# Performance work log

Hardware: AMD Instinct MI355X
Metric: run time of the kernel (lower is better)

Reference implementation:

```python
import jax, jax.numpy as jnp
import numpy as np

WS = 8      # window size
NH = 8      # num heads
DIM = 192


def _rel_coords_table(ws):
    c = np.arange(-(ws - 1), ws, dtype=np.float32)
    t = np.stack(np.meshgrid(c, c, indexing='ij'), axis=-1)  # (2ws-1, 2ws-1, 2)
    t = t / (ws - 1) * 8.0
    t = np.sign(t) * np.log2(np.abs(t) + 1.0) / np.log2(8.0)
    return jnp.asarray(t.reshape(-1, 2))


def _rel_pos_index(ws):
    coords = np.stack(np.meshgrid(np.arange(ws), np.arange(ws), indexing='ij'))  # (2,ws,ws)
    cf = coords.reshape(2, -1)
    rel = (cf[:, :, None] - cf[:, None, :]).transpose(1, 2, 0).astype(np.int64)  # (N,N,2)
    rel[..., 0] += ws - 1
    rel[..., 1] += ws - 1
    rel[..., 0] *= 2 * ws - 1
    return jnp.asarray(rel.sum(-1))  # (N,N)


_RCT = _rel_coords_table(WS)   # (225, 2)
_RPI = _rel_pos_index(WS)      # (64, 64)


def setup_inputs() -> dict:
    key = jax.random.key(0)
    ks = jax.random.split(key, 6)
    B, C, H, W = 4, DIM, 256, 256
    return {
        'x': jax.random.normal(ks[0], (B, C, H, W), dtype=jnp.float32),
        'img_alpha': jnp.ones((B, 1, H, W), dtype=jnp.float32),
        'qkv_w': jax.random.normal(ks[1], (3 * C, C), dtype=jnp.float32) * 0.02,
        'q_bias': jnp.zeros((C,), dtype=jnp.float32),
        'v_bias': jnp.zeros((C,), dtype=jnp.float32),
        'logit_scale': jnp.full((NH, 1, 1), np.log(10.0), dtype=jnp.float32),
        'cpb_w1': jax.random.normal(ks[2], (2, 512), dtype=jnp.float32) * 0.02,
        'cpb_b1': jnp.zeros((512,), dtype=jnp.float32),
        'cpb_w2': jax.random.normal(ks[3], (512, NH), dtype=jnp.float32) * 0.02,
        'proj_w': jax.random.normal(ks[4], (C, C), dtype=jnp.float32) * 0.02,
        'proj_b': jnp.zeros((C,), dtype=jnp.float32),
    }


def _forward(x, qkv_w, q_bias, v_bias, logit_scale, cpb_w1, cpb_b1, cpb_w2, proj_w, proj_b):
    B, C, H, W = x.shape
    ws, nh = WS, NH
    hd = C // nh
    # window partition: (B,C,H,W) -> (B*nW, N, C) with N = ws*ws
    xw = (x.transpose(0, 2, 3, 1)
           .reshape(B, H // ws, ws, W // ws, ws, C)
           .transpose(0, 1, 3, 2, 4, 5)
           .reshape(-1, ws * ws, C))
    Bw, N, _ = xw.shape
    # qkv with bias = [q_bias, 0, v_bias]
    qkv_b = jnp.concatenate([q_bias, jnp.zeros_like(v_bias), v_bias])
    qkv = (xw @ qkv_w.T + qkv_b).reshape(Bw, N, 3, nh, hd).transpose(2, 0, 3, 1, 4)
    q, k, v = qkv[0], qkv[1], qkv[2]  # (Bw, nh, N, hd)
    # cosine attention with clamped learnable logit scale
    qn = q / jnp.maximum(jnp.linalg.norm(q, axis=-1, keepdims=True), 1e-12)
    kn = k / jnp.maximum(jnp.linalg.norm(k, axis=-1, keepdims=True), 1e-12)
    scale = jnp.exp(jnp.minimum(logit_scale, jnp.log(jnp.float32(100.0))))  # (nh,1,1)
    attn = jnp.einsum('bhnd,bhmd->bhnm', qn, kn) * scale
    # relative position bias from small MLP + gather
    table = jax.nn.relu(_RCT @ cpb_w1 + cpb_b1) @ cpb_w2        # (225, nh)
    bias = table[_RPI.reshape(-1)].reshape(N, N, nh).transpose(2, 0, 1)  # (nh,N,N)
    bias = 16.0 * jax.nn.sigmoid(bias)
    attn = jax.nn.softmax(attn + bias[None], axis=-1)
    out = jnp.einsum('bhnm,bhmd->bhnd', attn, v).transpose(0, 2, 1, 3).reshape(Bw, N, C)
    out = out @ proj_w.T + proj_b
    # window reverse -> (B,C,H,W)
    out = (out.reshape(B, H // ws, W // ws, ws, ws, C)
              .transpose(0, 1, 3, 2, 4, 5)
              .reshape(B, H, W, C)
              .transpose(0, 3, 1, 2))
    return x + out  # residual (shortcut)


def reference(x, img_alpha, qkv_w, q_bias, v_bias, logit_scale,
              cpb_w1, cpb_b1, cpb_w2, proj_w, proj_b):
    # shift_size == 0: img_alpha only rides along through partition and is sliced off;
    # with all-ones alpha the zero-window removal is a no-op, so it does not affect output.
    del img_alpha
    return _forward(x, qkv_w, q_bias, v_bias, logit_scale,
                    cpb_w1, cpb_b1, cpb_w2, proj_w, proj_b)
```

## Files before the change

### kernel.cpp

```cpp
#include <hip/hip_runtime.h>

typedef unsigned short u16;
typedef __attribute__((ext_vector_type(8))) short bf16x8;
typedef __attribute__((ext_vector_type(4))) float f32x4;

#define C_    192
#define HW_   65536

__device__ inline u16 f2bf(float f) {
  union { float f; unsigned u; } x; x.f = f;
  unsigned r = x.u + 0x7FFFu + ((x.u >> 16) & 1u);
  return (u16)(r >> 16);
}
__device__ inline float bf2f(u16 s) {
  union { unsigned u; float f; } x; x.u = ((unsigned)s) << 16;
  return x.f;
}
__device__ inline unsigned pkbf(float lo, float hi) {
  unsigned r;
  asm("v_cvt_pk_bf16_f32 %0, %1, %2" : "=v"(r) : "v"(lo), "v"(hi));
  return r;
}

__global__ void k_convert(const float* __restrict__ qkv_w, const float* __restrict__ proj_w,
                          const float* __restrict__ q_bias, const float* __restrict__ v_bias,
                          u16* __restrict__ wq, u16* __restrict__ wp, float* __restrict__ qkvb) {
  int i = blockIdx.x * 256 + threadIdx.x;
  if (i < 110592) wq[i] = f2bf(qkv_w[i]);
  else if (i < 147456) wp[i - 110592] = f2bf(proj_w[i - 110592]);
  else if (i < 148032) {
    int j = i - 147456;
    qkvb[j] = (j < 192) ? q_bias[j] : ((j < 384) ? 0.f : v_bias[j - 384]);
  }
}

__global__ void k_table(const float* __restrict__ w1, const float* __restrict__ b1,
                        const float* __restrict__ w2, float* __restrict__ table) {
  int row = blockIdx.x;
  int tid = threadIdx.x;
  int a = row / 15, b = row % 15;
  float va = (float)(a - 7) * (8.0f / 7.0f);
  float vb = (float)(b - 7) * (8.0f / 7.0f);
  float c0 = copysignf(log2f(fabsf(va) + 1.0f) * (1.0f / 3.0f), va);
  float c1 = copysignf(log2f(fabsf(vb) + 1.0f) * (1.0f / 3.0f), vb);
  float acc[8];
#pragma unroll
  for (int o = 0; o < 8; ++o) acc[o] = 0.f;
  for (int k = tid; k < 512; k += 256) {
    float h = fmaxf(c0 * w1[k] + c1 * w1[512 + k] + b1[k], 0.f);
#pragma unroll
    for (int o = 0; o < 8; ++o) acc[o] += h * w2[k * 8 + o];
  }
  __shared__ float part[4][8];
  int wave = tid >> 6;
#pragma unroll
  for (int o = 0; o < 8; ++o) {
    float v = acc[o];
    v += __shfl_xor(v, 1, 64);  v += __shfl_xor(v, 2, 64);
    v += __shfl_xor(v, 4, 64);  v += __shfl_xor(v, 8, 64);
    v += __shfl_xor(v, 16, 64); v += __shfl_xor(v, 32, 64);
    acc[o] = v;
  }
  if ((tid & 63) == 0)
#pragma unroll
    for (int o = 0; o < 8; ++o) part[wave][o] = acc[o];
  __syncthreads();
  if (tid < 8)
    table[row * 8 + tid] = part[0][tid] + part[1][tid] + part[2][tid] + part[3][tid];
}

__global__ void k_biasfill(const float* __restrict__ table, float* __restrict__ bias3) {
  int p = blockIdx.x * 256 + threadIdx.x;
  int h = p >> 12, t = (p >> 6) & 63, g = (p >> 4) & 3, u = p & 15;
  int nt = u >> 2, r = u & 3;
  int s = nt * 16 + g * 4 + r;
  int idx = ((t >> 3) - (s >> 3) + 7) * 15 + ((t & 7) - (s & 7) + 7);
  float v = table[idx * 8 + h];
  bias3[p] = 16.0f / (1.0f + __expf(-v));
}

__device__ __forceinline__ void attn_window(
    u16* __restrict__ R0, u16* __restrict__ Sw, float* __restrict__ ikw,
    const u16* __restrict__ wq, const float* __restrict__ qkvb,
    const float* __restrict__ bias3,
    int h, int g, int li, float scaleh,
    const bf16x8* qw0, const bf16x8* qw1) {
  bf16x8 z8 = {0, 0, 0, 0, 0, 0, 0, 0};
  f32x4 zf = {0.f, 0.f, 0.f, 0.f};
  float iqr[4];
  bf16x8 qf[4], kf[4];

  {
    f32x4 cb0 = *(const f32x4*)(qkvb + h * 24 + g * 4);
    f32x4 cb1 = *(const f32x4*)(qkvb + h * 24 + 16 + g * 4);
#pragma unroll
    for (int tb = 0; tb < 4; ++tb) {
      int t = tb * 16 + li;
      bf16x8 xf[6];
#pragma unroll
      for (int ks = 0; ks < 6; ++ks)
        xf[ks] = *(const bf16x8*)&R0[t * 200 + ks * 32 + g * 8];
      f32x4 a0 = zf, a1 = zf;
#pragma unroll
      for (int ks = 0; ks < 6; ++ks) {
        a0 = __builtin_amdgcn_mfma_f32_16x16x32_bf16(qw0[ks], xf[ks], a0, 0, 0, 0);
        a1 = __builtin_amdgcn_mfma_f32_16x16x32_bf16(qw1[ks], xf[ks], a1, 0, 0, 0);
      }
      float p = 0.f;
#pragma unroll
      for (int r = 0; r < 4; ++r) { a0[r] += cb0[r]; p += a0[r] * a0[r]; }
      if (g < 2) {
#pragma unroll
        for (int r = 0; r < 4; ++r) { a1[r] += cb1[r]; p += a1[r] * a1[r]; }
      }
      p += __shfl_xor(p, 16, 64);
      p += __shfl_xor(p, 32, 64);
      iqr[tb] = __builtin_amdgcn_rsqf(fmaxf(p, 1e-24f)) * scaleh;
      uint2 pk;
      pk.x = pkbf(a0[0], a0[1]);
      pk.y = pkbf(a0[2], a0[3]);
      *(uint2*)&Sw[t * 24 + g * 4] = pk;
      if (g < 2) {
        pk.x = pkbf(a1[0], a1[1]);
        pk.y = pkbf(a1[2], a1[3]);
        *(uint2*)&Sw[t * 24 + 16 + g * 4] = pk;
      }
    }
  }

  bf16x8 kw0[6], kw1[6];
  {
    const u16* wr0 = wq + (size_t)(192 + h * 24 + li) * 192 + g * 8;
    const u16* wr1 = wq + (size_t)(192 + h * 24 + 16 + (li & 7)) * 192 + g * 8;
#pragma unroll
    for (int ks = 0; ks < 6; ++ks) {
      kw0[ks] = *(const bf16x8*)(wr0 + ks * 32);
      kw1[ks] = *(const bf16x8*)(wr1 + ks * 32);
    }
  }
#pragma unroll
  for (int tb = 0; tb < 4; ++tb)
    qf[tb] = (g < 3) ? *(const bf16x8*)&Sw[(tb * 16 + li) * 24 + g * 8] : z8;

  {
    f32x4 cb0 = *(const f32x4*)(qkvb + 192 + h * 24 + g * 4);
    f32x4 cb1 = *(const f32x4*)(qkvb + 192 + h * 24 + 16 + g * 4);
#pragma unroll
    for (int nt = 0; nt < 4; ++nt) {
      int t = nt * 16 + li;
      bf16x8 xf[6];
#pragma unroll
      for (int ks = 0; ks < 6; ++ks)
        xf[ks] = *(const bf16x8*)&R0[t * 200 + ks * 32 + g * 8];
      f32x4 a0 = zf, a1 = zf;
#pragma unroll
      for (int ks = 0; ks < 6; ++ks) {
        a0 = __builtin_amdgcn_mfma_f32_16x16x32_bf16(kw0[ks], xf[ks], a0, 0, 0, 0);
        a1 = __builtin_amdgcn_mfma_f32_16x16x32_bf16(kw1[ks], xf[ks], a1, 0, 0, 0);
      }
      float p = 0.f;
#pragma unroll
      for (int r = 0; r < 4; ++r) { a0[r] += cb0[r]; p += a0[r] * a0[r]; }
      if (g < 2) {
#pragma unroll
        for (int r = 0; r < 4; ++r) { a1[r] += cb1[r]; p += a1[r] * a1[r]; }
      }
      p += __shfl_xor(p, 16, 64);
      p += __shfl_xor(p, 32, 64);
      float ik = __builtin_amdgcn_rsqf(fmaxf(p, 1e-24f));
      if (g == 0) ikw[t] = ik;
      uint2 pk;
      pk.x = pkbf(a0[0], a0[1]);
      pk.y = pkbf(a0[2], a0[3]);
      *(uint2*)&Sw[t * 24 + g * 4] = pk;
      if (g < 2) {
        pk.x = pkbf(a1[0], a1[1]);
        pk.y = pkbf(a1[2], a1[3]);
        *(uint2*)&Sw[t * 24 + 16 + g * 4] = pk;
      }
    }
  }

  bf16x8 vw0[6], vw1[6];
  {
    const u16* wr0 = wq + (size_t)(384 + h * 24 + li) * 192 + g * 8;
    const u16* wr1 = wq + (size_t)(384 + h * 24 + 16 + (li & 7)) * 192 + g * 8;
#pragma unroll
    for (int ks = 0; ks < 6; ++ks) {
      vw0[ks] = *(const bf16x8*)(wr0 + ks * 32);
      vw1[ks] = *(const bf16x8*)(wr1 + ks * 32);
    }
  }
#pragma unroll
  for (int nt = 0; nt < 4; ++nt)
    kf[nt] = (g < 3) ? *(const bf16x8*)&Sw[(nt * 16 + li) * 24 + g * 8] : z8;

  {
    float vb0 = qkvb[384 + h * 24 + li];
    float vb1 = qkvb[384 + h * 24 + 16 + (li & 7)];
#pragma unroll
    for (int tb = 0; tb < 4; ++tb) {
      int t = tb * 16 + li;
      bf16x8 xf[6];
#pragma unroll
      for (int ks = 0; ks < 6; ++ks)
        xf[ks] = *(const bf16x8*)&R0[t * 200 + ks * 32 + g * 8];
      f32x4 a0 = zf, a1 = zf;
#pragma unroll
      for (int ks = 0; ks < 6; ++ks) {
        a0 = __builtin_amdgcn_mfma_f32_16x16x32_bf16(xf[ks], vw0[ks], a0, 0, 0, 0);
        a1 = __builtin_amdgcn_mfma_f32_16x16x32_bf16(xf[ks], vw1[ks], a1, 0, 0, 0);
      }
      uint2 pk;
      pk.x = pkbf(a0[0] + vb0, a0[1] + vb0);
      pk.y = pkbf(a0[2] + vb0, a0[3] + vb0);
      *(uint2*)&Sw[li * 72 + tb * 16 + g * 4] = pk;
      if (li < 8) {
        pk.x = pkbf(a1[0] + vb1, a1[1] + vb1);
        pk.y = pkbf(a1[2] + vb1, a1[3] + vb1);
        *(uint2*)&Sw[(16 + li) * 72 + tb * 16 + g * 4] = pk;
      }
    }
  }
  bf16x8 vf0[2], vf1[2];
#pragma unroll
  for (int ks = 0; ks < 2; ++ks) {
    vf0[ks] = *(const bf16x8*)&Sw[li * 72 + ks * 32 + g * 8];
    vf1[ks] = (li < 8) ? *(const bf16x8*)&Sw[(16 + li) * 72 + ks * 32 + g * 8] : z8;
  }

  f32x4 bx[2][4];
  {
    const float* bp0 = bias3 + ((h * 64 + li) << 6) + (g << 4);
#pragma unroll
    for (int nt = 0; nt < 4; ++nt) bx[0][nt] = *(const f32x4*)(bp0 + (nt << 2));
  }
#pragma unroll
  for (int tb = 0; tb < 4; ++tb) {
    if (tb < 3) {
      const float* bpn = bias3 + ((h * 64 + (tb + 1) * 16 + li) << 6) + (g << 4);
#pragma unroll
      for (int nt = 0; nt < 4; ++nt) bx[(tb + 1) & 1][nt] = *(const f32x4*)(bpn + (nt << 2));
    }
    f32x4 s4[4];
#pragma unroll
    for (int nt = 0; nt < 4; ++nt)
      s4[nt] = __builtin_amdgcn_mfma_f32_16x16x32_bf16(kf[nt], qf[tb], zf, 0, 0, 0);
    float iq = iqr[tb];
#pragma unroll
    for (int nt = 0; nt < 4; ++nt) {
      f32x4 ik4 = *(const f32x4*)&ikw[nt * 16 + g * 4];
#pragma unroll
      for (int r = 0; r < 4; ++r)
        s4[nt][r] = s4[nt][r] * iq * ik4[r] + bx[tb & 1][nt][r];
    }
    float m = s4[0][0];
#pragma unroll
    for (int nt = 0; nt < 4; ++nt)
#pragma unroll
      for (int r = 0; r < 4; ++r) m = fmaxf(m, s4[nt][r]);
    m = fmaxf(m, __shfl_xor(m, 16, 64));
    m = fmaxf(m, __shfl_xor(m, 32, 64));
    float sum = 0.f;
#pragma unroll
    for (int nt = 0; nt < 4; ++nt)
#pragma unroll
      for (int r = 0; r < 4; ++r) { float e = __expf(s4[nt][r] - m); s4[nt][r] = e; sum += e; }
    sum += __shfl_xor(sum, 16, 64);
    sum += __shfl_xor(sum, 32, 64);
    float is = __builtin_amdgcn_rcpf(sum);
#pragma unroll
    for (int nt = 0; nt < 4; ++nt) {
      uint2 pk;
      pk.x = pkbf(s4[nt][0], s4[nt][1]);
      pk.y = pkbf(s4[nt][2], s4[nt][3]);
      *(uint2*)&Sw[li * 72 + nt * 16 + g * 4] = pk;
    }
    f32x4 o0 = zf, o1 = zf;
#pragma unroll
    for (int ks = 0; ks < 2; ++ks) {
      bf16x8 pf = *(const bf16x8*)&Sw[li * 72 + ks * 32 + g * 8];
      o0 = __builtin_amdgcn_mfma_f32_16x16x32_bf16(vf0[ks], pf, o0, 0, 0, 0);
      o1 = __builtin_amdgcn_mfma_f32_16x16x32_bf16(vf1[ks], pf, o1, 0, 0, 0);
    }
    int t = tb * 16 + li;
    {
      uint2 pk;
      pk.x = pkbf(o0[0] * is, o0[1] * is);
      pk.y = pkbf(o0[2] * is, o0[3] * is);
      *(uint2*)&R0[t * 200 + h * 24 + g * 4] = pk;
    }
    if (g < 2) {
      uint2 pk;
      pk.x = pkbf(o1[0] * is, o1[1] * is);
      pk.y = pkbf(o1[2] * is, o1[3] * is);
      *(uint2*)&R0[t * 200 + h * 24 + 16 + g * 4] = pk;
    }
  }
}

__global__ __launch_bounds__(512, 2)
void k_main(const float* __restrict__ x,
            const float* __restrict__ ls, const float* __restrict__ proj_b,
            const u16* __restrict__ wq, const u16* __restrict__ wp,
            const float* __restrict__ qkvb, const float* __restrict__ bias3,
            float* __restrict__ out) {
  __shared__ u16 smem[40448];
  u16* R0A = smem;
  u16* R0B = smem + 12800;
  u16* Sc  = smem + 25600;
  float* ikwb = (float*)(smem + 39424);

  int tid  = threadIdx.x;
  int h = tid >> 6, lane = tid & 63, g = lane >> 4, li = lane & 15;
  int tt = h & 3, half = h >> 2;
  int bid = blockIdx.x;
  int b = bid >> 9, rem = bid & 511, wy = rem >> 4, wxp = rem & 15;
  const float* xb = x + (size_t)b * C_ * HW_;
  int baseA = (wy * 8) * 256 + wxp * 16;
  f32x4 zf = {0.f, 0.f, 0.f, 0.f};

  u16* Sw = Sc + h * 1728;
  float* ikw = ikwb + h * 64;
  float scaleh = __expf(fminf(ls[h], 4.6051702f));

  bf16x8 qwA0[6], qwA1[6];
  {
    const u16* wr0 = wq + (size_t)(h * 24 + li) * 192 + g * 8;
    const u16* wr1 = wq + (size_t)(h * 24 + 16 + (li & 7)) * 192 + g * 8;
#pragma unroll
    for (int ks = 0; ks < 6; ++ks) {
      qwA0[ks] = *(const bf16x8*)(wr0 + ks * 32);
      qwA1[ks] = *(const bf16x8*)(wr1 + ks * 32);
    }
  }

#pragma unroll
  for (int it = 0; it < 12; ++it) {
    int i4 = tid + it * 512;
    int c = i4 >> 5, r5 = i4 & 31;
    int ty = r5 >> 2, jq = (r5 & 3) * 4;
    float4 v = *(const float4*)(xb + c * HW_ + baseA + ty * 256 + jq);
    u16* Rw = (jq < 8) ? R0A : R0B;
    int t0 = ty * 8 + (jq & 7);
    unsigned p01 = pkbf(v.x, v.y), p23 = pkbf(v.z, v.w);
    Rw[(t0 + 0) * 200 + c] = (u16)p01;
    Rw[(t0 + 1) * 200 + c] = (u16)(p01 >> 16);
    Rw[(t0 + 2) * 200 + c] = (u16)p23;
    Rw[(t0 + 3) * 200 + c] = (u16)(p23 >> 16);
  }
  __syncthreads();

  attn_window(R0A, Sw, ikw, wq, qkvb, bias3, h, g, li, scaleh, qwA0, qwA1);

  bf16x8 qwB0[6], qwB1[6];
  {
    const u16* wr0 = wq + (size_t)(h * 24 + li) * 192 + g * 8;
    const u16* wr1 = wq + (size_t)(h * 24 + 16 + (li & 7)) * 192 + g * 8;
#pragma unroll
    for (int ks = 0; ks < 6; ++ks) {
      qwB0[ks] = *(const bf16x8*)(wr0 + ks * 32);
      qwB1[ks] = *(const bf16x8*)(wr1 + ks * 32);
    }
  }
  attn_window(R0B, Sw, ikw, wq, qkvb, bias3, h, g, li, scaleh, qwB0, qwB1);
  __syncthreads();

  bf16x8 afA[6], afB[6];
#pragma unroll
  for (int ks = 0; ks < 6; ++ks) {
    afA[ks] = *(const bf16x8*)&R0A[(tt * 16 + li) * 200 + ks * 32 + g * 8];
    afB[ks] = *(const bf16x8*)&R0B[(tt * 16 + li) * 200 + ks * 32 + g * 8];
  }
  __syncthreads();

  u16* obufA = Sc;
  u16* obufB = smem;
#pragma unroll
  for (int it = 0; it < 6; ++it) {
    int ct = half * 96 + it * 16;
    const u16* wr = wp + (size_t)(ct + li) * 192 + g * 8;
    bf16x8 w6[6];
#pragma unroll
    for (int ks = 0; ks < 6; ++ks) w6[ks] = *(const bf16x8*)(wr + ks * 32);
    f32x4 aA0 = zf, aA1 = zf, aB0 = zf, aB1 = zf;
#pragma unroll
    for (int ks = 0; ks < 3; ++ks) {
      aA0 = __builtin_amdgcn_mfma_f32_16x16x32_bf16(afA[ks], w6[ks], aA0, 0, 0, 0);
      aA1 = __builtin_amdgcn_mfma_f32_16x16x32_bf16(afA[ks + 3], w6[ks + 3], aA1, 0, 0, 0);
      aB0 = __builtin_amdgcn_mfma_f32_16x16x32_bf16(afB[ks], w6[ks], aB0, 0, 0, 0);
      aB1 = __builtin_amdgcn_mfma_f32_16x16x32_bf16(afB[ks + 3], w6[ks + 3], aB1, 0, 0, 0);
    }
    float pb = proj_b[ct + li];
    uint2 pk;
    pk.x = pkbf(aA0[0] + aA1[0] + pb, aA0[1] + aA1[1] + pb);
    pk.y = pkbf(aA0[2] + aA1[2] + pb, aA0[3] + aA1[3] + pb);
    *(uint2*)&obufA[(ct + li) * 68 + tt * 16 + g * 4] = pk;
    pk.x = pkbf(aB0[0] + aB1[0] + pb, aB0[1] + aB1[1] + pb);
    pk.y = pkbf(aB0[2] + aB1[2] + pb, aB0[3] + aB1[3] + pb);
    *(uint2*)&obufB[(ct + li) * 68 + tt * 16 + g * 4] = pk;
  }
  __syncthreads();

  float* ob = out + (size_t)b * C_ * HW_;
#pragma unroll
  for (int bt = 0; bt < 2; ++bt) {
    float4 xv[6];
    uint2 ov[6];
#pragma unroll
    for (int it = 0; it < 6; ++it) {
      int i4 = tid + (bt * 6 + it) * 512;
      int c = i4 >> 5, r5 = i4 & 31;
      int ty = r5 >> 2, jq = (r5 & 3) * 4;
      xv[it] = *(const float4*)(xb + c * HW_ + baseA + ty * 256 + jq);
    }
#pragma unroll
    for (int it = 0; it < 6; ++it) {
      int i4 = tid + (bt * 6 + it) * 512;
      int c = i4 >> 5, r5 = i4 & 31;
      int ty = r5 >> 2, jq = (r5 & 3) * 4;
      const u16* obw = (jq < 8) ? obufA : obufB;
      ov[it] = *(const uint2*)&obw[c * 68 + ty * 8 + (jq & 7)];
    }
#pragma unroll
    for (int it = 0; it < 6; ++it) {
      int i4 = tid + (bt * 6 + it) * 512;
      int c = i4 >> 5, r5 = i4 & 31;
      int ty = r5 >> 2, jq = (r5 & 3) * 4;
      float4 r;
      r.x = xv[it].x + bf2f((u16)(ov[it].x & 0xFFFFu));
      r.y = xv[it].y + bf2f((u16)(ov[it].x >> 16));
      r.z = xv[it].z + bf2f((u16)(ov[it].y & 0xFFFFu));
      r.w = xv[it].w + bf2f((u16)(ov[it].y >> 16));
      *(float4*)(ob + c * HW_ + baseA + ty * 256 + jq) = r;
    }
  }
}

extern "C" void kernel_launch(void* const* d_in, const int* in_sizes, int n_in,
                              void* d_out, int out_size, void* d_ws, size_t ws_size,
                              hipStream_t stream) {
  const float* x      = (const float*)d_in[0];
  const float* qkv_w  = (const float*)d_in[2];
  const float* q_bias = (const float*)d_in[3];
  const float* v_bias = (const float*)d_in[4];
  const float* ls     = (const float*)d_in[5];
  const float* w1     = (const float*)d_in[6];
  const float* b1     = (const float*)d_in[7];
  const float* w2     = (const float*)d_in[8];
  const float* proj_w = (const float*)d_in[9];
  const float* proj_b = (const float*)d_in[10];

  u16*   wq    = (u16*)d_ws;
  u16*   wpv   = wq + 110592;
  float* qkvb  = (float*)((char*)d_ws + 294912);
  float* bias3 = (float*)((char*)d_ws + 297216);
  float* table = (float*)((char*)d_ws + 428288);
  float* out   = (float*)d_out;

  hipLaunchKernelGGL(k_convert, dim3(579), dim3(256), 0, stream,
                     qkv_w, proj_w, q_bias, v_bias, wq, wpv, qkvb);
  hipLaunchKernelGGL(k_table, dim3(225), dim3(256), 0, stream, w1, b1, w2, table);
  hipLaunchKernelGGL(k_biasfill, dim3(128), dim3(256), 0, stream, table, bias3);
  hipLaunchKernelGGL(k_main, dim3(2048), dim3(512), 0, stream,
                     x, ls, proj_b, wq, wpv, qkvb, bias3, out);
}
```

Measured before the change: 415.4 us.

## Software-pipeline attention softmax with next tile and raise MFMA wave priority

```diff
diff --git a/kernel.cpp b/kernel.cpp
--- a/kernel.cpp
+++ b/kernel.cpp
@@ -101,11 +101,13 @@
       for (int ks = 0; ks < 6; ++ks)
         xf[ks] = *(const bf16x8*)&R0[t * 200 + ks * 32 + g * 8];
       f32x4 a0 = zf, a1 = zf;
+      __builtin_amdgcn_s_setprio(1);
 #pragma unroll
       for (int ks = 0; ks < 6; ++ks) {
         a0 = __builtin_amdgcn_mfma_f32_16x16x32_bf16(qw0[ks], xf[ks], a0, 0, 0, 0);
         a1 = __builtin_amdgcn_mfma_f32_16x16x32_bf16(qw1[ks], xf[ks], a1, 0, 0, 0);
       }
+      __builtin_amdgcn_s_setprio(0);
       float p = 0.f;
 #pragma unroll
       for (int r = 0; r < 4; ++r) { a0[r] += cb0[r]; p += a0[r] * a0[r]; }
@@ -153,11 +155,13 @@
       for (int ks = 0; ks < 6; ++ks)
         xf[ks] = *(const bf16x8*)&R0[t * 200 + ks * 32 + g * 8];
       f32x4 a0 = zf, a1 = zf;
+      __builtin_amdgcn_s_setprio(1);
 #pragma unroll
       for (int ks = 0; ks < 6; ++ks) {
         a0 = __builtin_amdgcn_mfma_f32_16x16x32_bf16(kw0[ks], xf[ks], a0, 0, 0, 0);
         a1 = __builtin_amdgcn_mfma_f32_16x16x32_bf16(kw1[ks], xf[ks], a1, 0, 0, 0);
       }
+      __builtin_amdgcn_s_setprio(0);
       float p = 0.f;
 #pragma unroll
       for (int r = 0; r < 4; ++r) { a0[r] += cb0[r]; p += a0[r] * a0[r]; }
@@ -206,11 +210,13 @@
       for (int ks = 0; ks < 6; ++ks)
         xf[ks] = *(const bf16x8*)&R0[t * 200 + ks * 32 + g * 8];
       f32x4 a0 = zf, a1 = zf;
+      __builtin_amdgcn_s_setprio(1);
 #pragma unroll
       for (int ks = 0; ks < 6; ++ks) {
         a0 = __builtin_amdgcn_mfma_f32_16x16x32_bf16(xf[ks], vw0[ks], a0, 0, 0, 0);
         a1 = __builtin_amdgcn_mfma_f32_16x16x32_bf16(xf[ks], vw1[ks], a1, 0, 0, 0);
       }
+      __builtin_amdgcn_s_setprio(0);
       uint2 pk;
       pk.x = pkbf(a0[0] + vb0, a0[1] + vb0);
       pk.y = pkbf(a0[2] + vb0, a0[3] + vb0);
@@ -229,30 +235,24 @@
     vf1[ks] = (li < 8) ? *(const bf16x8*)&Sw[(16 + li) * 72 + ks * 32 + g * 8] : z8;
   }
 
-  f32x4 bx[2][4];
-  {
-    const float* bp0 = bias3 + ((h * 64 + li) << 6) + (g << 4);
-#pragma unroll
-    for (int nt = 0; nt < 4; ++nt) bx[0][nt] = *(const f32x4*)(bp0 + (nt << 2));
-  }
-#pragma unroll
-  for (int tb = 0; tb < 4; ++tb) {
-    if (tb < 3) {
-      const float* bpn = bias3 + ((h * 64 + (tb + 1) * 16 + li) << 6) + (g << 4);
-#pragma unroll
-      for (int nt = 0; nt < 4; ++nt) bx[(tb + 1) & 1][nt] = *(const f32x4*)(bpn + (nt << 2));
-    }
+  auto compute_s = [&](int tb, uint2* pp) -> float {
+    f32x4 bxl[4];
+    const float* bp = bias3 + ((h * 64 + tb * 16 + li) << 6) + (g << 4);
+#pragma unroll
+    for (int nt = 0; nt < 4; ++nt) bxl[nt] = *(const f32x4*)(bp + (nt << 2));
     f32x4 s4[4];
+    __builtin_amdgcn_s_setprio(1);
 #pragma unroll
     for (int nt = 0; nt < 4; ++nt)
       s4[nt] = __builtin_amdgcn_mfma_f32_16x16x32_bf16(kf[nt], qf[tb], zf, 0, 0, 0);
+    __builtin_amdgcn_s_setprio(0);
     float iq = iqr[tb];
 #pragma unroll
     for (int nt = 0; nt < 4; ++nt) {
       f32x4 ik4 = *(const f32x4*)&ikw[nt * 16 + g * 4];
 #pragma unroll
       for (int r = 0; r < 4; ++r)
-        s4[nt][r] = s4[nt][r] * iq * ik4[r] + bx[tb & 1][nt][r];
+        s4[nt][r] = s4[nt][r] * iq * ik4[r] + bxl[nt][r];
     }
     float m = s4[0][0];
 #pragma unroll
@@ -268,33 +268,52 @@
       for (int r = 0; r < 4; ++r) { float e = __expf(s4[nt][r] - m); s4[nt][r] = e; sum += e; }
     sum += __shfl_xor(sum, 16, 64);
     sum += __shfl_xor(sum, 32, 64);
-    float is = __builtin_amdgcn_rcpf(sum);
 #pragma unroll
     for (int nt = 0; nt < 4; ++nt) {
-      uint2 pk;
-      pk.x = pkbf(s4[nt][0], s4[nt][1]);
-      pk.y = pkbf(s4[nt][2], s4[nt][3]);
-      *(uint2*)&Sw[li * 72 + nt * 16 + g * 4] = pk;
-    }
+      pp[nt].x = pkbf(s4[nt][0], s4[nt][1]);
+      pp[nt].y = pkbf(s4[nt][2], s4[nt][3]);
+    }
+    return __builtin_amdgcn_rcpf(sum);
+  };
+
+  uint2 pc[4];
+  float isc = compute_s(0, pc);
+#pragma unroll
+  for (int nt = 0; nt < 4; ++nt)
+    *(uint2*)&Sw[li * 72 + nt * 16 + g * 4] = pc[nt];
+
+#pragma unroll
+  for (int tb = 0; tb < 4; ++tb) {
+    uint2 pn[4];
+    float isn = 0.f;
+    if (tb < 3) isn = compute_s(tb + 1, pn);
     f32x4 o0 = zf, o1 = zf;
+    __builtin_amdgcn_s_setprio(1);
 #pragma unroll
     for (int ks = 0; ks < 2; ++ks) {
       bf16x8 pf = *(const bf16x8*)&Sw[li * 72 + ks * 32 + g * 8];
       o0 = __builtin_amdgcn_mfma_f32_16x16x32_bf16(vf0[ks], pf, o0, 0, 0, 0);
       o1 = __builtin_amdgcn_mfma_f32_16x16x32_bf16(vf1[ks], pf, o1, 0, 0, 0);
     }
+    __builtin_amdgcn_s_setprio(0);
     int t = tb * 16 + li;
     {
       uint2 pk;
-      pk.x = pkbf(o0[0] * is, o0[1] * is);
-      pk.y = pkbf(o0[2] * is, o0[3] * is);
+      pk.x = pkbf(o0[0] * isc, o0[1] * isc);
+      pk.y = pkbf(o0[2] * isc, o0[3] * isc);
       *(uint2*)&R0[t * 200 + h * 24 + g * 4] = pk;
     }
     if (g < 2) {
       uint2 pk;
-      pk.x = pkbf(o1[0] * is, o1[1] * is);
-      pk.y = pkbf(o1[2] * is, o1[3] * is);
+      pk.x = pkbf(o1[0] * isc, o1[1] * isc);
+      pk.y = pkbf(o1[2] * isc, o1[3] * isc);
       *(uint2*)&R0[t * 200 + h * 24 + 16 + g * 4] = pk;
+    }
+    if (tb < 3) {
+#pragma unroll
+      for (int nt = 0; nt < 4; ++nt)
+        *(uint2*)&Sw[li * 72 + nt * 16 + g * 4] = pn[nt];
+      isc = isn;
     }
   }
 }
@@ -384,6 +403,7 @@
 #pragma unroll
     for (int ks = 0; ks < 6; ++ks) w6[ks] = *(const bf16x8*)(wr + ks * 32);
     f32x4 aA0 = zf, aA1 = zf, aB0 = zf, aB1 = zf;
+    __builtin_amdgcn_s_setprio(1);
 #pragma unroll
     for (int ks = 0; ks < 3; ++ks) {
       aA0 = __builtin_amdgcn_mfma_f32_16x16x32_bf16(afA[ks], w6[ks], aA0, 0, 0, 0);
@@ -391,6 +411,7 @@
       aB0 = __builtin_amdgcn_mfma_f32_16x16x32_bf16(afB[ks], w6[ks], aB0, 0, 0, 0);
       aB1 = __builtin_amdgcn_mfma_f32_16x16x32_bf16(afB[ks + 3], w6[ks + 3], aB1, 0, 0, 0);
     }
+    __builtin_amdgcn_s_setprio(0);
     float pb = proj_b[ct + li];
     uint2 pk;
     pk.x = pkbf(aA0[0] + aA1[0] + pb, aA0[1] + aA1[1] + pb);
```

Measured after the change: 410.4 us (median of 2 runs). About the same (-1.2%).
